# Optimization experiments

Hardware: AMD Instinct MI355X
Metric: run time of the kernel (lower is better)

## Reference

```python
import jax, jax.numpy as jnp
import numpy as np

N, E, IN_DIM, HID = 50000, 1600000, 128, 64
NEG_SLOPE = 0.2  # PyG GATConv default negative_slope


def _gat_layer(x, src, dst, W, a_src, a_dst, b, heads, ch, n):
    # x: [n, f_in]; W: [f_in, heads*ch]; a_src/a_dst: [heads, ch]; b: [heads*ch]
    h = (x @ W).reshape(n, heads, ch)                 # [n, H, C]
    alpha_s = jnp.sum(h * a_src, axis=-1)             # [n, H]
    alpha_d = jnp.sum(h * a_dst, axis=-1)             # [n, H]
    e = jax.nn.leaky_relu(alpha_s[src] + alpha_d[dst], NEG_SLOPE)  # [E, H]
    # segment softmax over incoming edges of each dst node
    m = jax.ops.segment_max(e, dst, num_segments=n)   # [n, H]
    ex = jnp.exp(e - m[dst])
    denom = jax.ops.segment_sum(ex, dst, num_segments=n)
    alpha = ex / (denom[dst] + 1e-16)                 # [E, H]
    # scatter-add weighted source features
    out = jax.ops.segment_sum(h[src] * alpha[:, :, None], dst, num_segments=n)  # [n, H, C]
    return out.reshape(n, heads * ch) + b


def setup_inputs() -> dict:
    key = jax.random.key(0)
    ks = jax.random.split(key, 10)
    x = jax.random.normal(ks[0], (N, IN_DIM), dtype=jnp.float32)
    edge_index = jax.random.randint(ks[1], (2, E), 0, N, dtype=jnp.int32)
    s1 = 1.0 / np.sqrt(IN_DIM).astype(np.float32)
    W1 = jax.random.uniform(ks[2], (IN_DIM, 2 * HID), jnp.float32, -s1, s1)
    a_src1 = jax.random.uniform(ks[3], (2, HID), jnp.float32, -s1, s1)
    a_dst1 = jax.random.uniform(ks[4], (2, HID), jnp.float32, -s1, s1)
    b1 = jnp.zeros((2 * HID,), jnp.float32)
    s2 = 1.0 / np.sqrt(2 * HID).astype(np.float32)
    W2 = jax.random.uniform(ks[5], (2 * HID, 1), jnp.float32, -s2, s2)
    a_src2 = jax.random.uniform(ks[6], (1, 1), jnp.float32, -s2, s2)
    a_dst2 = jax.random.uniform(ks[7], (1, 1), jnp.float32, -s2, s2)
    b2 = jnp.zeros((1,), jnp.float32)
    return {"x": x, "edge_index": edge_index, "W1": W1, "a_src1": a_src1,
            "a_dst1": a_dst1, "b1": b1, "W2": W2, "a_src2": a_src2,
            "a_dst2": a_dst2, "b2": b2}


def reference(x, edge_index, W1, a_src1, a_dst1, b1, W2, a_src2, a_dst2, b2):
    n = x.shape[0]
    # PyG GATConv adds self-loops by default
    loops = jnp.arange(n, dtype=edge_index.dtype)
    src = jnp.concatenate([edge_index[0], loops])
    dst = jnp.concatenate([edge_index[1], loops])
    h = _gat_layer(x, src, dst, W1, a_src1, a_dst1, b1, heads=2, ch=HID, n=n)
    h = jax.nn.relu(h)
    out = _gat_layer(h, src, dst, W2, a_src2, a_dst2, b2, heads=1, ch=1, n=n)
    return jax.nn.sigmoid(out)  # [n, 1]
```

## Files before the change

kernel.cpp:

```cpp
#include <hip/hip_runtime.h>
#include <hip/hip_bf16.h>

#define LEAKY_SLOPE 0.2f

__device__ __forceinline__ float leaky(float x) { return x > 0.f ? x : LEAKY_SLOPE * x; }

__device__ __forceinline__ unsigned pack_bf16_pair(float lo, float hi)
{
    unsigned bl = __float_as_uint(lo);
    bl = (bl + 0x7fffu + ((bl >> 16) & 1u)) >> 16;
    unsigned bh = __float_as_uint(hi);
    bh = (bh + 0x7fffu + ((bh >> 16) & 1u)) & 0xffff0000u;
    return bl | bh;
}

__global__ __launch_bounds__(256) void gemm1_kernel(
    const float* __restrict__ x, const float* __restrict__ W1,
    const float* __restrict__ a_s, const float* __restrict__ a_d,
    unsigned* __restrict__ h1b, float2* __restrict__ as1, float2* __restrict__ ad1, int n)
{
    __shared__ float wlds[128 * 128];
    int tid = threadIdx.x;
    for (int i = tid; i < 128 * 128; i += 256) {
        int k = i >> 7, j = i & 127;
        wlds[(k << 7) + ((j & 63) * 2 + (j >> 6))] = W1[i];
    }
    int l  = tid & 31;
    int g  = tid >> 5;
    int p0 = l * 4;
    float aS[4], aD[4];
#pragma unroll
    for (int i = 0; i < 4; ++i) {
        int p = p0 + i;
        int j = ((p & 1) << 6) + (p >> 1);
        aS[i] = a_s[j];
        aD[i] = a_d[j];
    }
    __syncthreads();
    int lane = tid & 63;

    for (int base = blockIdx.x * 8; base < n; base += gridDim.x * 8) {
        int node = base + g;
        bool valid = node < n;
        float4 xr = make_float4(0.f, 0.f, 0.f, 0.f);
        if (valid) xr = *(const float4*)(x + (size_t)node * 128 + l * 4);
        float acc0 = 0.f, acc1 = 0.f, acc2 = 0.f, acc3 = 0.f;
#pragma unroll 8
        for (int k4 = 0; k4 < 32; ++k4) {
            int srcl = k4 + (lane & 32);
            float x0 = __shfl(xr.x, srcl);
            float x1 = __shfl(xr.y, srcl);
            float x2 = __shfl(xr.z, srcl);
            float x3 = __shfl(xr.w, srcl);
            const float4 w0 = *(const float4*)&wlds[(k4 * 4 + 0) * 128 + p0];
            const float4 w1 = *(const float4*)&wlds[(k4 * 4 + 1) * 128 + p0];
            const float4 w2 = *(const float4*)&wlds[(k4 * 4 + 2) * 128 + p0];
            const float4 w3 = *(const float4*)&wlds[(k4 * 4 + 3) * 128 + p0];
            acc0 = fmaf(x0, w0.x, acc0); acc1 = fmaf(x0, w0.y, acc1);
            acc2 = fmaf(x0, w0.z, acc2); acc3 = fmaf(x0, w0.w, acc3);
            acc0 = fmaf(x1, w1.x, acc0); acc1 = fmaf(x1, w1.y, acc1);
            acc2 = fmaf(x1, w1.z, acc2); acc3 = fmaf(x1, w1.w, acc3);
            acc0 = fmaf(x2, w2.x, acc0); acc1 = fmaf(x2, w2.y, acc1);
            acc2 = fmaf(x2, w2.z, acc2); acc3 = fmaf(x2, w2.w, acc3);
            acc0 = fmaf(x3, w3.x, acc0); acc1 = fmaf(x3, w3.y, acc1);
            acc2 = fmaf(x3, w3.z, acc2); acc3 = fmaf(x3, w3.w, acc3);
        }
        if (valid) {
            unsigned u0 = pack_bf16_pair(acc0, acc1);
            unsigned u1 = pack_bf16_pair(acc2, acc3);
            *(uint2*)&h1b[(size_t)node * 64 + 2 * l] = make_uint2(u0, u1);
            float vs0 = acc0 * aS[0] + acc2 * aS[2];
            float vs1 = acc1 * aS[1] + acc3 * aS[3];
            float vd0 = acc0 * aD[0] + acc2 * aD[2];
            float vd1 = acc1 * aD[1] + acc3 * aD[3];
#pragma unroll
            for (int off = 1; off < 32; off <<= 1) {
                vs0 += __shfl_xor(vs0, off);
                vs1 += __shfl_xor(vs1, off);
                vd0 += __shfl_xor(vd0, off);
                vd1 += __shfl_xor(vd1, off);
            }
            if (l == 0) {
                as1[node] = make_float2(vs0, vs1);
                ad1[node] = make_float2(vd0, vd1);
            }
        }
    }
}

#define CHUNK 8192

__global__ __launch_bounds__(256) void chist_kernel(
    const int* __restrict__ dst, int E, int NB, int NC, int* __restrict__ osc)
{
    __shared__ int h[256];
    int tid = threadIdx.x, c = blockIdx.x;
    h[tid] = 0;
    __syncthreads();
    int e0 = c * CHUNK, e1 = min(e0 + CHUNK, E);
    for (int e = e0 + tid; e < e1; e += 256)
        atomicAdd(&h[dst[e] >> 8], 1);
    __syncthreads();
    if (tid < NB) osc[tid * NC + c] = h[tid];
}

__global__ __launch_bounds__(1024) void oscan_kernel(int* __restrict__ osc, int len)
{
    __shared__ int wsum[16];
    int tid = threadIdx.x;
    int seg = (len + 1023) / 1024;
    int st = tid * seg, en = min(st + seg, len);
    int s = 0;
    for (int i = st; i < en; ++i) s += osc[i];
    int lane = tid & 63, w = tid >> 6;
    int incl = s;
#pragma unroll
    for (int off = 1; off < 64; off <<= 1) {
        int t = __shfl_up(incl, off);
        if (lane >= off) incl += t;
    }
    if (lane == 63) wsum[w] = incl;
    __syncthreads();
    int wb = 0;
    for (int i = 0; i < w; ++i) wb += wsum[i];
    int run = wb + incl - s;
    for (int i = st; i < en; ++i) { int v = osc[i]; osc[i] = run; run += v; }
}

__global__ __launch_bounds__(256) void cscatter_kernel(
    const int* __restrict__ src, const int* __restrict__ dst,
    int E, int NB, int NC, const int* __restrict__ osc, int2* __restrict__ pairs)
{
    __shared__ int cur[256];
    int tid = threadIdx.x, c = blockIdx.x;
    if (tid < NB) cur[tid] = osc[tid * NC + c];
    __syncthreads();
    int e0 = c * CHUNK, e1 = min(e0 + CHUNK, E);
    for (int e = e0 + tid; e < e1; e += 256) {
        int d = dst[e];
        int p = atomicAdd(&cur[d >> 8], 1);
        pairs[p] = make_int2(src[e], d);
    }
}

__global__ __launch_bounds__(256) void fsort_kernel(
    const int2* __restrict__ pairs, const int* __restrict__ osc,
    int E, int n, int NB, int NC,
    int* __restrict__ row_start, int* __restrict__ csr_src)
{
    __shared__ int fh[256];
    __shared__ int cur[256];
    __shared__ int wsum[4];
    int tid = threadIdx.x, b = blockIdx.x;
    int rbase = osc[b * NC];
    int rend  = (b + 1 < NB) ? osc[(b + 1) * NC] : E;
    fh[tid] = 0;
    __syncthreads();
    for (int i = rbase + tid; i < rend; i += 256)
        atomicAdd(&fh[pairs[i].y & 255], 1);
    __syncthreads();
    int v = fh[tid];
    int lane = tid & 63, w = tid >> 6;
    int incl = v;
#pragma unroll
    for (int off = 1; off < 64; off <<= 1) {
        int t = __shfl_up(incl, off);
        if (lane >= off) incl += t;
    }
    if (lane == 63) wsum[w] = incl;
    __syncthreads();
    int wb = 0;
    for (int i = 0; i < w; ++i) wb += wsum[i];
    int excl = wb + incl - v;
    int node = b * 256 + tid;
    if (node < n) row_start[node] = rbase + excl;
    cur[tid] = rbase + excl;
    __syncthreads();
    for (int i = rbase + tid; i < rend; i += 256) {
        int2 pr = pairs[i];
        int p = atomicAdd(&cur[pr.y & 255], 1);
        csr_src[p] = pr.x;
    }
    if (b == 0 && tid == 0) row_start[n] = E;
}

__global__ __launch_bounds__(256) void gather1_kernel(
    const unsigned* __restrict__ h1b, const float2* __restrict__ as1, const float2* __restrict__ ad1,
    const int* __restrict__ row_start, const int* __restrict__ csr_src,
    const float* __restrict__ b1, const float* __restrict__ W2,
    float* __restrict__ h2, int n)
{
    int wid = threadIdx.x >> 6, lane = threadIdx.x & 63;
    int v = blockIdx.x * 4 + wid;
    if (v >= n) return;

    float2 ad = ad1[v];
    float2 asv = as1[v];
    float m0 = leaky(asv.x + ad.x), m1 = leaky(asv.y + ad.y);
    float s0 = 1.f, s1 = 1.f;
    unsigned su = h1b[(size_t)v * 64 + lane];
    float acc0 = __uint_as_float(su << 16);
    float acc1 = __uint_as_float(su & 0xffff0000u);

    int t0 = row_start[v], t1 = row_start[v + 1];
    for (int t = t0; t < t1; t += 64) {
        int nv = t1 - t; if (nv > 64) nv = 64;
        int srcn = v;
        float e0 = -INFINITY, e1 = -INFINITY;
        if (lane < nv) {
            srcn = csr_src[t + lane];
            float2 as = as1[srcn];
            e0 = leaky(as.x + ad.x);
            e1 = leaky(as.y + ad.y);
        }
        float c0 = e0, c1 = e1;
#pragma unroll
        for (int off = 32; off >= 1; off >>= 1) {
            c0 = fmaxf(c0, __shfl_xor(c0, off));
            c1 = fmaxf(c1, __shfl_xor(c1, off));
        }
        float nm0 = fmaxf(m0, c0), nm1 = fmaxf(m1, c1);
        float r0 = __expf(m0 - nm0), r1 = __expf(m1 - nm1);
        acc0 *= r0; acc1 *= r1; s0 *= r0; s1 *= r1;
        m0 = nm0; m1 = nm1;
        float p0 = __expf(e0 - m0), p1 = __expf(e1 - m1);
        float q0 = p0, q1 = p1;
#pragma unroll
        for (int off = 32; off >= 1; off >>= 1) {
            q0 += __shfl_xor(q0, off);
            q1 += __shfl_xor(q1, off);
        }
        s0 += q0; s1 += q1;
        for (int j = 0; j < nv; ++j) {
            int sj   = __shfl(srcn, j);
            float w0 = __shfl(p0, j);
            float w1 = __shfl(p1, j);
            unsigned hu = h1b[(size_t)sj * 64 + lane];
            acc0 = fmaf(w0, __uint_as_float(hu << 16), acc0);
            acc1 = fmaf(w1, __uint_as_float(hu & 0xffff0000u), acc1);
        }
    }
    float o0 = acc0 / (s0 + 1e-16f) + b1[lane];
    float o1 = acc1 / (s1 + 1e-16f) + b1[64 + lane];
    o0 = fmaxf(o0, 0.f);
    o1 = fmaxf(o1, 0.f);
    float hv = o0 * W2[lane] + o1 * W2[64 + lane];
#pragma unroll
    for (int off = 1; off < 64; off <<= 1) hv += __shfl_xor(hv, off);
    if (lane == 0) h2[v] = hv;
}

__global__ void gather2_kernel(
    const float* __restrict__ h2, const int* __restrict__ row_start, const int* __restrict__ csr_src,
    const float* __restrict__ aS2, const float* __restrict__ aD2, const float* __restrict__ b2,
    float* __restrict__ out, int n)
{
    int v = blockIdx.x * 256 + threadIdx.x;
    if (v >= n) return;
    float as2 = aS2[0], ad2c = aD2[0];
    float hv = h2[v];
    float ad = hv * ad2c;
    float e = leaky(hv * as2 + ad);
    float m = e, s = 1.f, num = hv;
    int t1 = row_start[v + 1];
    for (int t = row_start[v]; t < t1; ++t) {
        int srcn = csr_src[t];
        float hsv = h2[srcn];
        float en = leaky(hsv * as2 + ad);
        if (en > m) { float c = __expf(m - en); s *= c; num *= c; m = en; }
        float p = __expf(en - m);
        s += p;
        num = fmaf(p, hsv, num);
    }
    float o = num / (s + 1e-16f) + b2[0];
    out[v] = 1.f / (1.f + __expf(-o));
}

extern "C" void kernel_launch(void* const* d_in, const int* in_sizes, int n_in,
                              void* d_out, int out_size, void* d_ws, size_t ws_size,
                              hipStream_t stream)
{
    const float* x      = (const float*)d_in[0];
    const int*   eidx   = (const int*)  d_in[1];
    const float* W1     = (const float*)d_in[2];
    const float* a_src1 = (const float*)d_in[3];
    const float* a_dst1 = (const float*)d_in[4];
    const float* b1     = (const float*)d_in[5];
    const float* W2     = (const float*)d_in[6];
    const float* a_src2 = (const float*)d_in[7];
    const float* a_dst2 = (const float*)d_in[8];
    const float* b2     = (const float*)d_in[9];

    int n = in_sizes[0] / 128;
    int E = in_sizes[1] / 2;
    const int* src = eidx;
    const int* dst = eidx + E;

    int NC = (E + CHUNK - 1) / CHUNK;
    int NB = (n + 255) / 256;

    char* ws = (char*)d_ws;
    size_t off = 0;
    auto alloc = [&](size_t bytes) { size_t o = off; off += (bytes + 255) & ~(size_t)255; return o; };

    unsigned* h1b    = (unsigned*)(ws + alloc((size_t)n * 64 * 4));
    float2* as1     = (float2*)(ws + alloc((size_t)n * 8));
    float2* ad1     = (float2*)(ws + alloc((size_t)n * 8));
    float*  h2      = (float*) (ws + alloc((size_t)n * 4));
    int*    rowst   = (int*)   (ws + alloc((size_t)(n + 1) * 4));
    int*    osc     = (int*)   (ws + alloc((size_t)NB * NC * 4));
    int2*   pairs   = (int2*)  (ws + alloc((size_t)E * 8));
    int*    csr_src = (int*)   (ws + alloc((size_t)E * 4));
    (void)ws_size; (void)n_in; (void)out_size;

    gemm1_kernel<<<1024, 256, 0, stream>>>(x, W1, a_src1, a_dst1, h1b, as1, ad1, n);

    chist_kernel<<<NC, 256, 0, stream>>>(dst, E, NB, NC, osc);
    oscan_kernel<<<1, 1024, 0, stream>>>(osc, NB * NC);
    cscatter_kernel<<<NC, 256, 0, stream>>>(src, dst, E, NB, NC, osc, pairs);
    fsort_kernel<<<NB, 256, 0, stream>>>(pairs, osc, E, n, NB, NC, rowst, csr_src);

    gather1_kernel<<<(n + 3) / 4, 256, 0, stream>>>(h1b, as1, ad1, rowst, csr_src, b1, W2, h2, n);
    gather2_kernel<<<(n + 255) / 256, 256, 0, stream>>>(h2, rowst, csr_src, a_src2, a_dst2, b2,
                                                        (float*)d_out, n);
}
```

Measured before the change: 386.3 us.

## Use global max bound for softmax and vectorize gather with 16-lane edge groups

Computes a global upper bound on the source attention logits (the max of alpha_src) during the GEMM and passes it via atomicMax keys, so the per-node softmax can skip the online max rescaling and warp-wide max reductions. The gather kernel now has four 16-lane groups each process a different edge with uint4 loads of bf16 features, and packs the weights to fp16 for the shuffles. Layer 2 uses a similar min/max bound on h2. This cuts shuffles and reductions per edge and raises memory-level parallelism, but adds fp16 weight rounding and the risk of exp underflow when the global bound is far above a node's local max.

Result: slower. 1.449 ms (+275.0%).

```diff
diff --git a/kernel.cpp b/kernel.cpp
--- a/kernel.cpp
+++ b/kernel.cpp
@@ -1,25 +1,42 @@
 #include <hip/hip_runtime.h>
 #include <hip/hip_bf16.h>
+#include <hip/hip_fp16.h>
 
 #define LEAKY_SLOPE 0.2f
 
 __device__ __forceinline__ float leaky(float x) { return x > 0.f ? x : LEAKY_SLOPE * x; }
 
+__device__ __forceinline__ unsigned fkey(float f)
+{
+    unsigned u = __float_as_uint(f);
+    return (u & 0x80000000u) ? ~u : (u | 0x80000000u);
+}
+__device__ __forceinline__ float key_to_float(unsigned k)
+{
+    unsigned u = (k & 0x80000000u) ? (k & 0x7fffffffu) : ~k;
+    return __uint_as_float(u);
+}
+
+__device__ __forceinline__ float bl(unsigned u) { return __uint_as_float(u << 16); }
+__device__ __forceinline__ float bh(unsigned u) { return __uint_as_float(u & 0xffff0000u); }
+
 __device__ __forceinline__ unsigned pack_bf16_pair(float lo, float hi)
 {
-    unsigned bl = __float_as_uint(lo);
-    bl = (bl + 0x7fffu + ((bl >> 16) & 1u)) >> 16;
-    unsigned bh = __float_as_uint(hi);
-    bh = (bh + 0x7fffu + ((bh >> 16) & 1u)) & 0xffff0000u;
-    return bl | bh;
+    unsigned blv = __float_as_uint(lo);
+    blv = (blv + 0x7fffu + ((blv >> 16) & 1u)) >> 16;
+    unsigned bhv = __float_as_uint(hi);
+    bhv = (bhv + 0x7fffu + ((bhv >> 16) & 1u)) & 0xffff0000u;
+    return blv | bhv;
 }
 
 __global__ __launch_bounds__(256) void gemm1_kernel(
     const float* __restrict__ x, const float* __restrict__ W1,
     const float* __restrict__ a_s, const float* __restrict__ a_d,
-    unsigned* __restrict__ h1b, float2* __restrict__ as1, float2* __restrict__ ad1, int n)
+    unsigned* __restrict__ h1b, float2* __restrict__ as1, float2* __restrict__ ad1,
+    unsigned* __restrict__ keys, int n)
 {
     __shared__ float wlds[128 * 128];
+    __shared__ float smax0[8], smax1[8];
     int tid = threadIdx.x;
     for (int i = tid; i < 128 * 128; i += 256) {
         int k = i >> 7, j = i & 127;
@@ -38,6 +55,7 @@
     }
     __syncthreads();
     int lane = tid & 63;
+    float rmax0 = -INFINITY, rmax1 = -INFINITY;
 
     for (int base = blockIdx.x * 8; base < n; base += gridDim.x * 8) {
         int node = base + g;
@@ -83,8 +101,19 @@
             if (l == 0) {
                 as1[node] = make_float2(vs0, vs1);
                 ad1[node] = make_float2(vd0, vd1);
+                rmax0 = fmaxf(rmax0, vs0);
+                rmax1 = fmaxf(rmax1, vs1);
             }
         }
+    }
+    if (l == 0) { smax0[g] = rmax0; smax1[g] = rmax1; }
+    __syncthreads();
+    if (tid == 0) {
+        float m0 = smax0[0], m1 = smax1[0];
+#pragma unroll
+        for (int i = 1; i < 8; ++i) { m0 = fmaxf(m0, smax0[i]); m1 = fmaxf(m1, smax1[i]); }
+        atomicMax(&keys[0], fkey(m0));
+        atomicMax(&keys[1], fkey(m1));
     }
 }
 
@@ -188,89 +217,119 @@
     const unsigned* __restrict__ h1b, const float2* __restrict__ as1, const float2* __restrict__ ad1,
     const int* __restrict__ row_start, const int* __restrict__ csr_src,
     const float* __restrict__ b1, const float* __restrict__ W2,
-    float* __restrict__ h2, int n)
+    unsigned* __restrict__ keys, float* __restrict__ h2, int n)
 {
     int wid = threadIdx.x >> 6, lane = threadIdx.x & 63;
     int v = blockIdx.x * 4 + wid;
     if (v >= n) return;
+    int grp = lane >> 4, li = lane & 15;
+
+    float gm0 = key_to_float(keys[0]);
+    float gm1 = key_to_float(keys[1]);
 
     float2 ad = ad1[v];
     float2 asv = as1[v];
-    float m0 = leaky(asv.x + ad.x), m1 = leaky(asv.y + ad.y);
-    float s0 = 1.f, s1 = 1.f;
-    unsigned su = h1b[(size_t)v * 64 + lane];
-    float acc0 = __uint_as_float(su << 16);
-    float acc1 = __uint_as_float(su & 0xffff0000u);
+    float m0 = leaky(gm0 + ad.x), m1 = leaky(gm1 + ad.y);
+    float ps0 = __expf(leaky(asv.x + ad.x) - m0);
+    float ps1 = __expf(leaky(asv.y + ad.y) - m1);
+
+    float a0x = 0.f, a0y = 0.f, a0z = 0.f, a0w = 0.f;
+    float a1x = 0.f, a1y = 0.f, a1z = 0.f, a1w = 0.f;
+    if (grp == 0) {
+        uint4 hu = *(const uint4*)&h1b[(size_t)v * 64 + li * 4];
+        a0x = ps0 * bl(hu.x); a1x = ps1 * bh(hu.x);
+        a0y = ps0 * bl(hu.y); a1y = ps1 * bh(hu.y);
+        a0z = ps0 * bl(hu.z); a1z = ps1 * bh(hu.z);
+        a0w = ps0 * bl(hu.w); a1w = ps1 * bh(hu.w);
+    }
+    float s0l = 0.f, s1l = 0.f;
 
     int t0 = row_start[v], t1 = row_start[v + 1];
     for (int t = t0; t < t1; t += 64) {
         int nv = t1 - t; if (nv > 64) nv = 64;
         int srcn = v;
-        float e0 = -INFINITY, e1 = -INFINITY;
+        float p0 = 0.f, p1 = 0.f;
         if (lane < nv) {
             srcn = csr_src[t + lane];
             float2 as = as1[srcn];
-            e0 = leaky(as.x + ad.x);
-            e1 = leaky(as.y + ad.y);
+            p0 = __expf(leaky(as.x + ad.x) - m0);
+            p1 = __expf(leaky(as.y + ad.y) - m1);
         }
-        float c0 = e0, c1 = e1;
-#pragma unroll
-        for (int off = 32; off >= 1; off >>= 1) {
-            c0 = fmaxf(c0, __shfl_xor(c0, off));
-            c1 = fmaxf(c1, __shfl_xor(c1, off));
+        s0l += p0; s1l += p1;
+        int pk = (int)__builtin_bit_cast(unsigned, __floats2half2_rn(p0, p1));
+        int jmax = (nv + 3) >> 2;
+        for (int j = 0; j < jmax; ++j) {
+            int idx = 4 * j + grp;
+            int sj = __shfl(srcn, idx);
+            __half2 hp = __builtin_bit_cast(__half2, (unsigned)__shfl(pk, idx));
+            float w0 = __half2float(__low2half(hp));
+            float w1 = __half2float(__high2half(hp));
+            uint4 hu = *(const uint4*)&h1b[(size_t)sj * 64 + li * 4];
+            a0x = fmaf(w0, bl(hu.x), a0x); a1x = fmaf(w1, bh(hu.x), a1x);
+            a0y = fmaf(w0, bl(hu.y), a0y); a1y = fmaf(w1, bh(hu.y), a1y);
+            a0z = fmaf(w0, bl(hu.z), a0z); a1z = fmaf(w1, bh(hu.z), a1z);
+            a0w = fmaf(w0, bl(hu.w), a0w); a1w = fmaf(w1, bh(hu.w), a1w);
         }
-        float nm0 = fmaxf(m0, c0), nm1 = fmaxf(m1, c1);
-        float r0 = __expf(m0 - nm0), r1 = __expf(m1 - nm1);
-        acc0 *= r0; acc1 *= r1; s0 *= r0; s1 *= r1;
-        m0 = nm0; m1 = nm1;
-        float p0 = __expf(e0 - m0), p1 = __expf(e1 - m1);
-        float q0 = p0, q1 = p1;
-#pragma unroll
-        for (int off = 32; off >= 1; off >>= 1) {
-            q0 += __shfl_xor(q0, off);
-            q1 += __shfl_xor(q1, off);
-        }
-        s0 += q0; s1 += q1;
-        for (int j = 0; j < nv; ++j) {
-            int sj   = __shfl(srcn, j);
-            float w0 = __shfl(p0, j);
-            float w1 = __shfl(p1, j);
-            unsigned hu = h1b[(size_t)sj * 64 + lane];
-            acc0 = fmaf(w0, __uint_as_float(hu << 16), acc0);
-            acc1 = fmaf(w1, __uint_as_float(hu & 0xffff0000u), acc1);
-        }
-    }
-    float o0 = acc0 / (s0 + 1e-16f) + b1[lane];
-    float o1 = acc1 / (s1 + 1e-16f) + b1[64 + lane];
-    o0 = fmaxf(o0, 0.f);
-    o1 = fmaxf(o1, 0.f);
-    float hv = o0 * W2[lane] + o1 * W2[64 + lane];
-#pragma unroll
-    for (int off = 1; off < 64; off <<= 1) hv += __shfl_xor(hv, off);
-    if (lane == 0) h2[v] = hv;
+    }
+#pragma unroll
+    for (int off = 32; off >= 1; off >>= 1) {
+        s0l += __shfl_xor(s0l, off);
+        s1l += __shfl_xor(s1l, off);
+    }
+    float inv0 = 1.f / (s0l + ps0 + 1e-16f);
+    float inv1 = 1.f / (s1l + ps1 + 1e-16f);
+#pragma unroll
+    for (int off = 16; off <= 32; off <<= 1) {
+        a0x += __shfl_xor(a0x, off); a1x += __shfl_xor(a1x, off);
+        a0y += __shfl_xor(a0y, off); a1y += __shfl_xor(a1y, off);
+        a0z += __shfl_xor(a0z, off); a1z += __shfl_xor(a1z, off);
+        a0w += __shfl_xor(a0w, off); a1w += __shfl_xor(a1w, off);
+    }
+    const float4 b0v = *(const float4*)&b1[4 * li];
+    const float4 b1v = *(const float4*)&b1[64 + 4 * li];
+    const float4 w0v = *(const float4*)&W2[4 * li];
+    const float4 w1v = *(const float4*)&W2[64 + 4 * li];
+    float o;
+    float hv = 0.f;
+    o = fmaxf(fmaf(a0x, inv0, b0v.x), 0.f); hv = fmaf(o, w0v.x, hv);
+    o = fmaxf(fmaf(a0y, inv0, b0v.y), 0.f); hv = fmaf(o, w0v.y, hv);
+    o = fmaxf(fmaf(a0z, inv0, b0v.z), 0.f); hv = fmaf(o, w0v.z, hv);
+    o = fmaxf(fmaf(a0w, inv0, b0v.w), 0.f); hv = fmaf(o, w0v.w, hv);
+    o = fmaxf(fmaf(a1x, inv1, b1v.x), 0.f); hv = fmaf(o, w1v.x, hv);
+    o = fmaxf(fmaf(a1y, inv1, b1v.y), 0.f); hv = fmaf(o, w1v.y, hv);
+    o = fmaxf(fmaf(a1z, inv1, b1v.z), 0.f); hv = fmaf(o, w1v.z, hv);
+    o = fmaxf(fmaf(a1w, inv1, b1v.w), 0.f); hv = fmaf(o, w1v.w, hv);
+#pragma unroll
+    for (int off = 1; off <= 8; off <<= 1) hv += __shfl_xor(hv, off);
+    if (lane == 0) {
+        h2[v] = hv;
+        atomicMax(&keys[2], fkey(hv));
+        atomicMin(&keys[3], fkey(hv));
+    }
 }
 
 __global__ void gather2_kernel(
     const float* __restrict__ h2, const int* __restrict__ row_start, const int* __restrict__ csr_src,
     const float* __restrict__ aS2, const float* __restrict__ aD2, const float* __restrict__ b2,
-    float* __restrict__ out, int n)
+    const unsigned* __restrict__ keys, float* __restrict__ out, int n)
 {
     int v = blockIdx.x * 256 + threadIdx.x;
     if (v >= n) return;
     float as2 = aS2[0], ad2c = aD2[0];
+    float hmax = key_to_float(keys[2]);
+    float hmin = key_to_float(keys[3]);
+    float B = as2 >= 0.f ? as2 * hmax : as2 * hmin;
     float hv = h2[v];
     float ad = hv * ad2c;
-    float e = leaky(hv * as2 + ad);
-    float m = e, s = 1.f, num = hv;
+    float m = leaky(B + ad);
+    float ps = __expf(leaky(fmaf(hv, as2, ad)) - m);
+    float s = ps, num = ps * hv;
     int t1 = row_start[v + 1];
     for (int t = row_start[v]; t < t1; ++t) {
-        int srcn = csr_src[t];
-        float hsv = h2[srcn];
-        float en = leaky(hsv * as2 + ad);
-        if (en > m) { float c = __expf(m - en); s *= c; num *= c; m = en; }
-        float p = __expf(en - m);
+        float hs = h2[csr_src[t]];
+        float p = __expf(leaky(fmaf(hs, as2, ad)) - m);
         s += p;
-        num = fmaf(p, hsv, num);
+        num = fmaf(p, hs, num);
     }
     float o = num / (s + 1e-16f) + b2[0];
     out[v] = 1.f / (1.f + __expf(-o));
@@ -303,24 +362,29 @@
     size_t off = 0;
     auto alloc = [&](size_t bytes) { size_t o = off; off += (bytes + 255) & ~(size_t)255; return o; };
 
-    unsigned* h1b    = (unsigned*)(ws + alloc((size_t)n * 64 * 4));
+    unsigned* h1b   = (unsigned*)(ws + alloc((size_t)n * 64 * 4));
     float2* as1     = (float2*)(ws + alloc((size_t)n * 8));
     float2* ad1     = (float2*)(ws + alloc((size_t)n * 8));
     float*  h2      = (float*) (ws + alloc((size_t)n * 4));
     int*    rowst   = (int*)   (ws + alloc((size_t)(n + 1) * 4));
+    unsigned* keys  = (unsigned*)(ws + alloc(4 * 4));
     int*    osc     = (int*)   (ws + alloc((size_t)NB * NC * 4));
     int2*   pairs   = (int2*)  (ws + alloc((size_t)E * 8));
     int*    csr_src = (int*)   (ws + alloc((size_t)E * 4));
     (void)ws_size; (void)n_in; (void)out_size;
 
-    gemm1_kernel<<<1024, 256, 0, stream>>>(x, W1, a_src1, a_dst1, h1b, as1, ad1, n);
+    hipMemsetAsync(keys, 0x00, 12, stream);
+    hipMemsetAsync(keys + 3, 0xFF, 4, stream);
+
+    gemm1_kernel<<<1024, 256, 0, stream>>>(x, W1, a_src1, a_dst1, h1b, as1, ad1, keys, n);
 
     chist_kernel<<<NC, 256, 0, stream>>>(dst, E, NB, NC, osc);
     oscan_kernel<<<1, 1024, 0, stream>>>(osc, NB * NC);
     cscatter_kernel<<<NC, 256, 0, stream>>>(src, dst, E, NB, NC, osc, pairs);
     fsort_kernel<<<NB, 256, 0, stream>>>(pairs, osc, E, n, NB, NC, rowst, csr_src);
 
-    gather1_kernel<<<(n + 3) / 4, 256, 0, stream>>>(h1b, as1, ad1, rowst, csr_src, b1, W2, h2, n);
+    gather1_kernel<<<(n + 3) / 4, 256, 0, stream>>>(h1b, as1, ad1, rowst, csr_src, b1, W2,
+                                                    keys, h2, n);
     gather2_kernel<<<(n + 255) / 256, 256, 0, stream>>>(h2, rowst, csr_src, a_src2, a_dst2, b2,
-                                                        (float*)d_out, n);
-}
+                                                        keys, (float*)d_out, n);
+}
```
